# Kernel optimization log

Measured on AMD Instinct MI355X. Metric: run time of the kernel, lower is better.

The kernel has to match this reference:

```python
import jax, jax.numpy as jnp
import numpy as np

N = 100_000      # nodes
DEG = 16         # avg in-degree (fixed per node for setup)
E = N * DEG      # edges
IN = 256         # in_feats
H = 4            # num_heads
D = 64           # out_feats per head
NEG_SLOPE = 0.2


def setup_inputs() -> dict:
    key = jax.random.key(0)
    k1, k2, k3, k4, k5 = jax.random.split(key, 5)
    # dst-major CSR with uniform degree DEG per destination node
    row_ptr = jnp.arange(N + 1, dtype=jnp.int32) * DEG          # [N+1]
    col_ind = jax.random.randint(k1, (E,), 0, N, dtype=jnp.int32)  # source ids per edge
    feat = jax.random.normal(k2, (N, IN), dtype=jnp.float32)
    # fc.weight (xavier-ish scale), torch Linear: y = x @ W.T
    W = jax.random.normal(k3, (H * D, IN), dtype=jnp.float32) * (1.0 / np.sqrt(IN))
    attn_l = jax.random.normal(k4, (1, H, D), dtype=jnp.float32) * 0.1
    attn_r = jax.random.normal(k5, (1, H, D), dtype=jnp.float32) * 0.1
    return {"row_ptr": row_ptr, "col_ind": col_ind, "feat": feat,
            "W": W, "attn_l": attn_l, "attn_r": attn_r}


def reference(row_ptr, col_ind, feat, W, attn_l, attn_r):
    n_nodes = feat.shape[0]
    n_edges = col_ind.shape[0]
    # feat_src = feat_dst = fc(feat).view(-1, H, D)
    feat_src = (feat @ W.T).reshape(n_nodes, H, D)
    el = jnp.sum(feat_src * attn_l, axis=-1)   # [N, H]
    er = jnp.sum(feat_src * attn_r, axis=-1)   # [N, H]
    # per-edge dst id from CSR row_ptr; src = col_ind
    dst = (jnp.searchsorted(row_ptr, jnp.arange(n_edges, dtype=row_ptr.dtype),
                            side='right') - 1).astype(jnp.int32)
    src = col_ind
    # e = u_add_v(g, er, el) -> er[src] + el[dst], then LeakyReLU
    e = er[src] + el[dst]                      # [E, H]
    e = jnp.where(e > 0, e, NEG_SLOPE * e)
    # CSR edge-softmax: normalize over incoming edges of each dst row
    m = jax.ops.segment_max(e, dst, num_segments=n_nodes)    # [N, H]
    ex = jnp.exp(e - m[dst])
    s = jax.ops.segment_sum(ex, dst, num_segments=n_nodes)   # [N, H]
    a = ex / s[dst]                                          # [E, H]
    # multi-head SpMM: out[n,h] = sum_{e: dst=n} a[e,h] * feat_src[src[e],h]
    outs = []
    for h in range(H):  # small fixed head loop to avoid [E,H,D] intermediate
        msg = a[:, h, None] * feat_src[src, h]               # [E, D]
        outs.append(jax.ops.segment_sum(msg, dst, num_segments=n_nodes))
    return jnp.stack(outs, axis=1)                           # [N, H, D]
```

## Files before the change

### kernel.cpp

```cpp
#include <hip/hip_runtime.h>
#include <math.h>


#define HEADS 4
#define KIN 256
#define NOUT 256
#define NEG_SLOPE 0.2f
#define BK 32
#define SA 40
#define SB 40

typedef __attribute__((ext_vector_type(4))) short short4v;
typedef __attribute__((ext_vector_type(8))) short short8v;
typedef __attribute__((ext_vector_type(4))) float floatx4;

static __device__ __forceinline__ unsigned short f2bf(float x) {
  unsigned u = __float_as_uint(x);
  u += 0x7FFFu + ((u >> 16) & 1u);
  return (unsigned short)(u >> 16);
}
static __device__ __forceinline__ float bf2f(unsigned short b) {
  return __uint_as_float(((unsigned)b) << 16);
}

__global__ __launch_bounds__(256) void k_cast_w(const float* __restrict__ W,
                                                unsigned short* __restrict__ Wbf) {
  const int i = blockIdx.x * 256 + threadIdx.x;
  float4 f = ((const float4*)W)[i];
  ushort4 o;
  o.x = f2bf(f.x); o.y = f2bf(f.y); o.z = f2bf(f.z); o.w = f2bf(f.w);
  ((ushort4*)Wbf)[i] = o;
}

__global__ __launch_bounds__(256) void k_gemm_mfma(
    const float* __restrict__ feat, const unsigned short* __restrict__ Wbf,
    const float* __restrict__ attn_l, const float* __restrict__ attn_r,
    unsigned short* __restrict__ fs_bf, float* __restrict__ el,
    float* __restrict__ er, int n_nodes) {
  __shared__ unsigned short Alds[64 * SA];
  __shared__ unsigned short Blds[256 * SB];

  const int tid = threadIdx.x;
  const int lane = tid & 63;
  const int w = tid >> 6;
  const int m0 = blockIdx.x * 64;
  const int q = lane >> 4;
  const int l15 = lane & 15;

  floatx4 acc[4][4];
#pragma unroll
  for (int mt = 0; mt < 4; ++mt)
#pragma unroll
    for (int nt = 0; nt < 4; ++nt)
#pragma unroll
      for (int r = 0; r < 4; ++r) acc[mt][nt][r] = 0.0f;

  const int a_row = tid >> 3;
  const int a_kk = (tid & 7) * 4;

  for (int kc = 0; kc < 8; ++kc) {
    const int k0 = kc * BK;
#pragma unroll
    for (int half = 0; half < 2; ++half) {
      const int row = a_row + half * 32;
      int gr = m0 + row;
      if (gr >= n_nodes) gr = n_nodes - 1;
      float4 f = *(const float4*)(feat + (size_t)gr * KIN + k0 + a_kk);
      uint2 p;
      p.x = ((unsigned)f2bf(f.y) << 16) | f2bf(f.x);
      p.y = ((unsigned)f2bf(f.w) << 16) | f2bf(f.z);
      *(uint2*)(&Alds[row * SA + a_kk]) = p;
    }
    {
      const uint4* src = (const uint4*)(Wbf + (size_t)tid * KIN + k0);
      uint2* dst = (uint2*)(&Blds[tid * SB]);
#pragma unroll
      for (int i = 0; i < 4; ++i) {
        uint4 v = src[i];
        dst[2 * i + 0] = make_uint2(v.x, v.y);
        dst[2 * i + 1] = make_uint2(v.z, v.w);
      }
    }
    __syncthreads();
    short8v af[4], bfr[4];
#pragma unroll
    for (int mt = 0; mt < 4; ++mt) {
      const unsigned short* p = &Alds[(mt * 16 + l15) * SA + q * 8];
      short4v lo = *(const short4v*)p;
      short4v hi = *(const short4v*)(p + 4);
      af[mt] = __builtin_shufflevector(lo, hi, 0, 1, 2, 3, 4, 5, 6, 7);
    }
#pragma unroll
    for (int nt = 0; nt < 4; ++nt) {
      const unsigned short* p = &Blds[(w * 64 + nt * 16 + l15) * SB + q * 8];
      short4v lo = *(const short4v*)p;
      short4v hi = *(const short4v*)(p + 4);
      bfr[nt] = __builtin_shufflevector(lo, hi, 0, 1, 2, 3, 4, 5, 6, 7);
    }
#pragma unroll
    for (int mt = 0; mt < 4; ++mt)
#pragma unroll
      for (int nt = 0; nt < 4; ++nt)
        acc[mt][nt] = __builtin_amdgcn_mfma_f32_16x16x32_bf16(
            af[mt], bfr[nt], acc[mt][nt], 0, 0, 0);
    __syncthreads();
  }

  float alv[4], arv[4];
#pragma unroll
  for (int nt = 0; nt < 4; ++nt) {
    alv[nt] = attn_l[w * 64 + nt * 16 + l15];
    arv[nt] = attn_r[w * 64 + nt * 16 + l15];
  }
#pragma unroll
  for (int mt = 0; mt < 4; ++mt) {
#pragma unroll
    for (int r = 0; r < 4; ++r) {
      const int m = m0 + mt * 16 + q * 4 + r;
      const bool mvalid = (m < n_nodes);
      float pl = 0.f, pr = 0.f;
#pragma unroll
      for (int nt = 0; nt < 4; ++nt) {
        const float v = acc[mt][nt][r];
        pl = fmaf(v, alv[nt], pl);
        pr = fmaf(v, arv[nt], pr);
        if (mvalid)
          fs_bf[(size_t)m * NOUT + w * 64 + nt * 16 + l15] = f2bf(v);
      }
#pragma unroll
      for (int off = 1; off < 16; off <<= 1) {
        pl += __shfl_xor(pl, off, 64);
        pr += __shfl_xor(pr, off, 64);
      }
      if (l15 == 0 && mvalid) {
        el[m * HEADS + w] = pl;
        er[m * HEADS + w] = pr;
      }
    }
  }
}

__global__ __launch_bounds__(256, 4) void k_aggregate(
    const int* __restrict__ row_ptr, const int* __restrict__ col_ind,
    const float* __restrict__ el, const float* __restrict__ er,
    const unsigned short* __restrict__ fs_bf, float* __restrict__ out,
    int n_nodes) {
  const int gid = blockIdx.x * blockDim.x + threadIdx.x;
  const int node = gid >> 6;
  const int lane = threadIdx.x & 63;
  if (node >= n_nodes) return;

  const int h = lane >> 4;
  const int j = lane & 15;
  const int rs = row_ptr[node];
  const int deg = row_ptr[node + 1] - rs;

  const bool valid = (j < deg);
  const int src = valid ? col_ind[rs + j] : 0;

  float e = valid ? (er[src * HEADS + h] + el[node * HEADS + h]) : -INFINITY;
  e = (e > 0.f) ? e : NEG_SLOPE * e;

  float mx = e;
#pragma unroll
  for (int off = 1; off < 16; off <<= 1) mx = fmaxf(mx, __shfl_xor(mx, off, 64));
  float ex = valid ? __expf(e - mx) : 0.f;
  float s = ex;
#pragma unroll
  for (int off = 1; off < 16; off <<= 1) s += __shfl_xor(s, off, 64);
  const float a = ex / s;

  const int half = lane >> 5;
  const int li = lane & 31;
  const int hd = li >> 3;

  int sj[8];
#pragma unroll
  for (int p = 0; p < 8; ++p) sj[p] = __shfl(src, 2 * p + half, 64);

  uint4 u[8];
#pragma unroll
  for (int p = 0; p < 8; ++p)
    u[p] = ((const uint4*)(fs_bf + (size_t)sj[p] * NOUT))[li];

  float wgt[8];
#pragma unroll
  for (int p = 0; p < 8; ++p)
    wgt[p] = __shfl(a, hd * 16 + 2 * p + half, 64);

  float acc[8];
#pragma unroll
  for (int k = 0; k < 8; ++k) acc[k] = 0.f;
#pragma unroll
  for (int p = 0; p < 8; ++p) {
    const uint4 v = u[p];
    const float w0 = wgt[p];
    acc[0] = fmaf(w0, __uint_as_float(v.x << 16), acc[0]);
    acc[1] = fmaf(w0, __uint_as_float(v.x & 0xFFFF0000u), acc[1]);
    acc[2] = fmaf(w0, __uint_as_float(v.y << 16), acc[2]);
    acc[3] = fmaf(w0, __uint_as_float(v.y & 0xFFFF0000u), acc[3]);
    acc[4] = fmaf(w0, __uint_as_float(v.z << 16), acc[4]);
    acc[5] = fmaf(w0, __uint_as_float(v.z & 0xFFFF0000u), acc[5]);
    acc[6] = fmaf(w0, __uint_as_float(v.w << 16), acc[6]);
    acc[7] = fmaf(w0, __uint_as_float(v.w & 0xFFFF0000u), acc[7]);
  }

#pragma unroll
  for (int k = 0; k < 8; ++k) acc[k] += __shfl_xor(acc[k], 32, 64);

  float4 o;
  o.x = half ? acc[4] : acc[0];
  o.y = half ? acc[5] : acc[1];
  o.z = half ? acc[6] : acc[2];
  o.w = half ? acc[7] : acc[3];
  *(float4*)(out + (size_t)node * NOUT + li * 8 + half * 4) = o;
}

extern "C" void kernel_launch(void* const* d_in, const int* in_sizes, int n_in,
                              void* d_out, int out_size, void* d_ws, size_t ws_size,
                              hipStream_t stream) {
  const int* row_ptr = (const int*)d_in[0];
  const int* col_ind = (const int*)d_in[1];
  const float* feat = (const float*)d_in[2];
  const float* W = (const float*)d_in[3];
  const float* attn_l = (const float*)d_in[4];
  const float* attn_r = (const float*)d_in[5];
  float* out = (float*)d_out;
  const int n_nodes = in_sizes[0] - 1;

  char* ws = (char*)d_ws;
  unsigned short* Wbf = (unsigned short*)ws;
  unsigned short* fs_bf = (unsigned short*)(ws + 128 * 1024);
  size_t fs_bytes = (size_t)n_nodes * NOUT * sizeof(unsigned short);
  float* el = (float*)(ws + 128 * 1024 + fs_bytes);
  float* er = el + (size_t)n_nodes * HEADS;

  k_cast_w<<<64, 256, 0, stream>>>(W, Wbf);
  k_gemm_mfma<<<(n_nodes + 63) / 64, 256, 0, stream>>>(
      feat, Wbf, attn_l, attn_r, fs_bf, el, er, n_nodes);
  k_aggregate<<<(n_nodes + 3) / 4, 256, 0, stream>>>(
      row_ptr, col_ind, el, er, fs_bf, out, n_nodes);
}
```

Measured before the change: 360.0 us.

## Pre-cast features to bf16 and stream GEMM A tiles via direct global-to-LDS loads

A separate cast kernel now converts the whole feature matrix and W to bf16, staging the feature copy in the output buffer. The GEMM loads A tiles straight into swizzled, double-buffered LDS with global_load_lds, and reads W fragments directly from global memory instead of from LDS. The point is to halve the bytes the GEMM reads, overlap the next tile's load with the current MFMAs, and shrink LDS use (launch bounds now ask for 3 blocks per SM). In exchange it adds a full extra pass that writes and re-reads the bf16 features, plus uncached-LDS W loads from global memory.

Measured after the change: 368.3 us. 1.02x slower.

```diff
diff --git a/kernel.cpp b/kernel.cpp
--- a/kernel.cpp
+++ b/kernel.cpp
@@ -6,9 +6,6 @@
 #define KIN 256
 #define NOUT 256
 #define NEG_SLOPE 0.2f
-#define BK 32
-#define SA 40
-#define SB 40
 
 typedef __attribute__((ext_vector_type(4))) short short4v;
 typedef __attribute__((ext_vector_type(8))) short short8v;
@@ -23,22 +20,32 @@
   return __uint_as_float(((unsigned)b) << 16);
 }
 
-__global__ __launch_bounds__(256) void k_cast_w(const float* __restrict__ W,
-                                                unsigned short* __restrict__ Wbf) {
-  const int i = blockIdx.x * 256 + threadIdx.x;
-  float4 f = ((const float4*)W)[i];
-  ushort4 o;
-  o.x = f2bf(f.x); o.y = f2bf(f.y); o.z = f2bf(f.z); o.w = f2bf(f.w);
-  ((ushort4*)Wbf)[i] = o;
-}
-
-__global__ __launch_bounds__(256) void k_gemm_mfma(
-    const float* __restrict__ feat, const unsigned short* __restrict__ Wbf,
+__global__ __launch_bounds__(256) void k_cast(
+    const float* __restrict__ feat, const float* __restrict__ W,
+    unsigned short* __restrict__ feat_bf, unsigned short* __restrict__ Wbf,
+    int n4) {
+  const int stride = gridDim.x * 256;
+  for (int i = blockIdx.x * 256 + threadIdx.x; i < n4; i += stride) {
+    float4 f = ((const float4*)feat)[i];
+    ushort4 o;
+    o.x = f2bf(f.x); o.y = f2bf(f.y); o.z = f2bf(f.z); o.w = f2bf(f.w);
+    ((ushort4*)feat_bf)[i] = o;
+    if (i < (NOUT * KIN / 4)) {
+      float4 g = ((const float4*)W)[i];
+      ushort4 p;
+      p.x = f2bf(g.x); p.y = f2bf(g.y); p.z = f2bf(g.z); p.w = f2bf(g.w);
+      ((ushort4*)Wbf)[i] = p;
+    }
+  }
+}
+
+__global__ __launch_bounds__(256, 3) void k_gemm_mfma(
+    const unsigned short* __restrict__ feat_bf,
+    const unsigned short* __restrict__ Wbf,
     const float* __restrict__ attn_l, const float* __restrict__ attn_r,
     unsigned short* __restrict__ fs_bf, float* __restrict__ el,
     float* __restrict__ er, int n_nodes) {
-  __shared__ unsigned short Alds[64 * SA];
-  __shared__ unsigned short Blds[256 * SB];
+  __shared__ unsigned short Alds[2][64 * 64];
 
   const int tid = threadIdx.x;
   const int lane = tid & 63;
@@ -55,55 +62,52 @@
 #pragma unroll
       for (int r = 0; r < 4; ++r) acc[mt][nt][r] = 0.0f;
 
-  const int a_row = tid >> 3;
-  const int a_kk = (tid & 7) * 4;
-
-  for (int kc = 0; kc < 8; ++kc) {
-    const int k0 = kc * BK;
-#pragma unroll
-    for (int half = 0; half < 2; ++half) {
-      const int row = a_row + half * 32;
+  const int rsub = lane >> 3;
+  const int gg = lane & 7;
+  const int sg = gg ^ rsub;
+
+  auto stage = [&](int kc, int b) {
+#pragma unroll
+    for (int s = 0; s < 2; ++s) {
+      const int row = w * 16 + s * 8 + rsub;
       int gr = m0 + row;
       if (gr >= n_nodes) gr = n_nodes - 1;
-      float4 f = *(const float4*)(feat + (size_t)gr * KIN + k0 + a_kk);
-      uint2 p;
-      p.x = ((unsigned)f2bf(f.y) << 16) | f2bf(f.x);
-      p.y = ((unsigned)f2bf(f.w) << 16) | f2bf(f.z);
-      *(uint2*)(&Alds[row * SA + a_kk]) = p;
-    }
-    {
-      const uint4* src = (const uint4*)(Wbf + (size_t)tid * KIN + k0);
-      uint2* dst = (uint2*)(&Blds[tid * SB]);
-#pragma unroll
-      for (int i = 0; i < 4; ++i) {
-        uint4 v = src[i];
-        dst[2 * i + 0] = make_uint2(v.x, v.y);
-        dst[2 * i + 1] = make_uint2(v.z, v.w);
-      }
-    }
+      const unsigned short* src = feat_bf + (size_t)gr * KIN + kc * 64 + sg * 8;
+      unsigned short* dst = &Alds[b][(w * 16 + s * 8) * 64];
+      __builtin_amdgcn_global_load_lds(
+          (const __attribute__((address_space(1))) unsigned int*)src,
+          (__attribute__((address_space(3))) unsigned int*)dst, 16, 0, 0);
+    }
+  };
+
+  stage(0, 0);
+  for (int kc = 0; kc < 4; ++kc) {
     __syncthreads();
-    short8v af[4], bfr[4];
-#pragma unroll
-    for (int mt = 0; mt < 4; ++mt) {
-      const unsigned short* p = &Alds[(mt * 16 + l15) * SA + q * 8];
-      short4v lo = *(const short4v*)p;
-      short4v hi = *(const short4v*)(p + 4);
-      af[mt] = __builtin_shufflevector(lo, hi, 0, 1, 2, 3, 4, 5, 6, 7);
-    }
-#pragma unroll
-    for (int nt = 0; nt < 4; ++nt) {
-      const unsigned short* p = &Blds[(w * 64 + nt * 16 + l15) * SB + q * 8];
-      short4v lo = *(const short4v*)p;
-      short4v hi = *(const short4v*)(p + 4);
-      bfr[nt] = __builtin_shufflevector(lo, hi, 0, 1, 2, 3, 4, 5, 6, 7);
-    }
-#pragma unroll
-    for (int mt = 0; mt < 4; ++mt)
+    if (kc < 3) stage(kc + 1, (kc + 1) & 1);
+
+    short8v bfr[2][4];
+#pragma unroll
+    for (int ks = 0; ks < 2; ++ks)
 #pragma unroll
       for (int nt = 0; nt < 4; ++nt)
-        acc[mt][nt] = __builtin_amdgcn_mfma_f32_16x16x32_bf16(
-            af[mt], bfr[nt], acc[mt][nt], 0, 0, 0);
-    __syncthreads();
+        bfr[ks][nt] = *(const short8v*)(Wbf + (size_t)(w * 64 + nt * 16 + l15) * KIN +
+                                        kc * 64 + ks * 32 + q * 8);
+
+#pragma unroll
+    for (int ks = 0; ks < 2; ++ks) {
+      short8v af[4];
+#pragma unroll
+      for (int mt = 0; mt < 4; ++mt) {
+        const int slot = (ks * 4 + q) ^ (l15 & 7);
+        af[mt] = *(const short8v*)(&Alds[kc & 1][(mt * 16 + l15) * 64 + slot * 8]);
+      }
+#pragma unroll
+      for (int mt = 0; mt < 4; ++mt)
+#pragma unroll
+        for (int nt = 0; nt < 4; ++nt)
+          acc[mt][nt] = __builtin_amdgcn_mfma_f32_16x16x32_bf16(
+              af[mt], bfr[ks][nt], acc[mt][nt], 0, 0, 0);
+    }
   }
 
   float alv[4], arv[4];
@@ -235,9 +239,11 @@
   float* el = (float*)(ws + 128 * 1024 + fs_bytes);
   float* er = el + (size_t)n_nodes * HEADS;
 
-  k_cast_w<<<64, 256, 0, stream>>>(W, Wbf);
+  unsigned short* feat_bf = (unsigned short*)d_out;
+
+  k_cast<<<2048, 256, 0, stream>>>(feat, W, feat_bf, Wbf, n_nodes * (KIN / 4));
   k_gemm_mfma<<<(n_nodes + 63) / 64, 256, 0, stream>>>(
-      feat, Wbf, attn_l, attn_r, fs_bf, el, er, n_nodes);
+      feat_bf, Wbf, attn_l, attn_r, fs_bf, el, er, n_nodes);
   k_aggregate<<<(n_nodes + 3) / 4, 256, 0, stream>>>(
       row_ptr, col_ind, el, er, fs_bf, out, n_nodes);
 }
```
